# Kernel optimization log

Hardware: AMD Instinct MI355X
Metric: run time of the kernel (lower is better)

## Reference

```python
import jax, jax.numpy as jnp
import numpy as np
from jax import lax

B, N, C = 4, 20000, 256
NUM_VIEW = 300
NUM_SAMPLE = 1024
EPS_BN = 1e-5


def _grasp_views(n=NUM_VIEW):
    # graspnetAPI generate_grasp_views: spiral points on unit sphere
    phi = (np.sqrt(5.0) - 1.0) / 2.0
    i = np.arange(n)
    z = (2.0 * i + 1.0) / n - 1.0
    r = np.sqrt(np.maximum(1.0 - z * z, 0.0))
    x = r * np.cos(2.0 * np.pi * i * phi)
    y = r * np.sin(2.0 * np.pi * i * phi)
    return jnp.asarray(np.stack([x, y, z], axis=1).astype(np.float32))  # [300,3]

_TEMPLATE_VIEWS = _grasp_views()


def _conv1x1(x, w, b):
    # Conv1d with kernel_size=1: x [B,Cin,N], w [Cout,Cin], b [Cout]
    return jnp.einsum('oc,bcn->bon', w, x) + b[None, :, None]


def _bn_eval(x, g, be, m, v):
    # BatchNorm1d in eval mode (running stats)
    scale = g / jnp.sqrt(v + EPS_BN)
    return x * scale[None, :, None] + (be - m * scale)[None, :, None]


def _masked_fps(xyz, mask, n_samples):
    # Equivalent to compacting valid points, running torch furthest_point_sample,
    # and mapping indices back: run FPS on the full set with invalid points pinned
    # to -inf min-distance so they are never selected. Start = first valid index
    # (index 0 of the compacted set). Tie-breaking matches (order preserved).
    first = jnp.argmax(mask, axis=1)                      # [B]
    init_d = jnp.where(mask, jnp.float32(1e10), -jnp.inf)  # [B,N]

    def step(carry, _):
        dists, last = carry
        p = jnp.take_along_axis(xyz, last[:, None, None], axis=1)  # [B,1,3]
        d = jnp.sum((xyz - p) ** 2, axis=-1)                       # [B,N]
        dists = jnp.minimum(dists, d)
        nxt = jnp.argmax(dists, axis=1)
        return (dists, nxt), nxt

    _, rest = lax.scan(step, (init_d, first), None, length=n_samples - 1)
    return jnp.concatenate([first[None, :], rest], axis=0).T  # [B,S] int


def _viewpoint_to_matrix(towards):
    # batch_viewpoint_params_to_matrix with batch_angle = 0 => R1 = I
    ax = towards  # [M,3]
    ay = jnp.stack([-ax[:, 1], ax[:, 0], jnp.zeros_like(ax[:, 0])], axis=-1)
    deg = jnp.sum(ay * ay, axis=-1, keepdims=True) == 0
    ay = jnp.where(deg, jnp.array([0.0, 1.0, 0.0], dtype=ax.dtype), ay)
    nx = ax / jnp.linalg.norm(ax, axis=-1, keepdims=True)
    ny = ay / jnp.linalg.norm(ay, axis=-1, keepdims=True)
    nz = jnp.cross(nx, ny)
    return jnp.stack([nx, ny, nz], axis=-1)  # [M,3,3], axes as columns


def setup_inputs() -> dict:
    key = jax.random.key(0)
    ks = jax.random.split(key, 18)

    def w(k, shape, s=0.05):
        return jax.random.normal(k, shape, jnp.float32) * s

    return dict(
        seed_xyz=jax.random.normal(ks[0], (B, N, 3), jnp.float32),
        seed_features=jax.random.normal(ks[1], (B, C, N), jnp.float32),
        gh_w1=w(ks[2], (C, C)), gh_b1=w(ks[3], (C,), 0.01),
        gh_g=1.0 + 0.1 * jax.random.normal(ks[4], (C,), jnp.float32),
        gh_be=w(ks[5], (C,), 0.01),
        gh_m=w(ks[6], (C,), 0.1),
        gh_v=jax.random.uniform(ks[7], (C,), jnp.float32, 0.5, 1.5),
        gh_w2=w(ks[8], (3, C)), gh_b2=w(ks[9], (3,), 0.01),
        c1_w=w(ks[10], (C, C)), c1_b=w(ks[11], (C,), 0.01),
        bn_g=1.0 + 0.1 * jax.random.normal(ks[12], (C,), jnp.float32),
        bn_b=w(ks[13], (C,), 0.01),
        bn_m=w(ks[14], (C,), 0.1),
        bn_v=jax.random.uniform(ks[15], (C,), jnp.float32, 0.5, 1.5),
        c2_w=w(ks[16], (3, C)), c2_b=w(ks[17], (3,), 0.01),
    )


def reference(seed_xyz, seed_features, gh_w1, gh_b1, gh_g, gh_be, gh_m, gh_v,
              gh_w2, gh_b2, c1_w, c1_b, bn_g, bn_b, bn_m, bn_v, c2_w, c2_b):
    # graspable head: conv-BN-ReLU-conv -> [B,3,N]
    h = jax.nn.relu(_bn_eval(_conv1x1(seed_features, gh_w1, gh_b1), gh_g, gh_be, gh_m, gh_v))
    graspable = _conv1x1(h, gh_w2, gh_b2)
    objectness_score = graspable[:, :2]          # [B,2,N]
    graspness_score = graspable[:, 2]            # [B,N]

    obj_mask = jnp.argmax(objectness_score, axis=1) == 1
    gmask = (graspness_score > 0.1) & obj_mask   # [B,N] bool

    graspable_inds = _masked_fps(seed_xyz, gmask, NUM_SAMPLE)            # [B,S]
    graspable_xyz = jnp.take_along_axis(seed_xyz, graspable_inds[:, :, None], axis=1)   # [B,S,3]
    graspable_features = jnp.take_along_axis(seed_features, graspable_inds[:, None, :], axis=2)  # [B,C,S]
    fp2_graspness = jnp.take_along_axis(graspness_score, graspable_inds, axis=1)        # [B,S]

    f = jax.nn.relu(_bn_eval(_conv1x1(graspable_features, c1_w, c1_b), bn_g, bn_b, bn_m, bn_v))
    vp_xyz = jnp.transpose(_conv1x1(f, c2_w, c2_b), (0, 2, 1))  # [B,S,3]

    # cosine similarity against 300 template views (torch clamps each norm at 1e-8)
    vn = vp_xyz / jnp.maximum(jnp.linalg.norm(vp_xyz, axis=-1, keepdims=True), 1e-8)
    tn = _TEMPLATE_VIEWS / jnp.maximum(jnp.linalg.norm(_TEMPLATE_VIEWS, axis=-1, keepdims=True), 1e-8)
    cos = jnp.einsum('bsd,vd->bsv', vn, tn)      # [B,S,300]
    top_view_inds = jnp.argmax(cos, axis=2)      # [B,S]

    vp_rot = _viewpoint_to_matrix(-vp_xyz.reshape(-1, 3)).reshape(B, NUM_SAMPLE, 3, 3)

    return (objectness_score, graspness_score, graspable_xyz, graspable_inds,
            graspable_features, fp2_graspness, vp_xyz, top_view_inds, vp_rot)
```

## Files before the change

### kernel.cpp

```cpp
#include <hip/hip_runtime.h>
#include <hip/hip_bf16.h>
#include <math.h>

static constexpr int BB = 4;
static constexpr int NN = 20000;
static constexpr int CC = 256;
static constexpr int SS = 1024;
static constexpr int NV = 300;

static constexpr size_t O0 = 0;
static constexpr size_t O1 = O0 + (size_t)BB*2*NN;
static constexpr size_t O2 = O1 + (size_t)BB*NN;
static constexpr size_t O3 = O2 + (size_t)BB*SS*3;
static constexpr size_t O4 = O3 + (size_t)BB*SS;
static constexpr size_t O5 = O4 + (size_t)BB*CC*SS;
static constexpr size_t O6 = O5 + (size_t)BB*SS;
static constexpr size_t O7 = O6 + (size_t)BB*SS*3;
static constexpr size_t O8 = O7 + (size_t)BB*SS;

typedef float v2f __attribute__((ext_vector_type(2)));

static constexpr int TN = 64;
static constexpr int KC = 32;
static constexpr int SW_LD = 260;
static constexpr int PS_LD = 68;

static constexpr int G1_TN  = 64;
static constexpr int G1_KC  = 16;
static constexpr int G1_LD  = 260;
static constexpr int G1_BUF = G1_KC*G1_LD + G1_KC*G1_TN;

__global__ __launch_bounds__(256, 2) void gemm_fused(
    const float* __restrict__ X,
    const float* __restrict__ W1, const float* __restrict__ B1v,
    const float* __restrict__ Gv, const float* __restrict__ BEv,
    const float* __restrict__ Mv, const float* __restrict__ Vv,
    const float* __restrict__ W2, const float* __restrict__ B2v,
    float* __restrict__ o0, float* __restrict__ o1)
{
    __shared__ alignas(16) float smem[2*G1_BUF];
    float* psum = smem;
    float* gout = smem + 3*32*PS_LD;

    const int t  = threadIdx.x;
    const int b  = blockIdx.y;
    const int n0 = blockIdx.x * G1_TN;
    const int tm = t & 31;
    const int tn = t >> 5;
    const float* Xb = X + (size_t)b * CC * NN;
    const bool full = (n0 + G1_TN <= NN);

    v2f acc2[8][4];
#pragma unroll
    for (int i = 0; i < 8; ++i)
#pragma unroll
        for (int jp = 0; jp < 4; ++jp) acc2[i][jp] = (v2f){0.f, 0.f};

    float4 wreg[4];
    float4 xreg;

    auto stage_load = [&](int k0) {
#pragma unroll
        for (int r = 0; r < 4; ++r) {
            int f  = r*1024 + t*4;
            int m  = f >> 4;
            int kk = f & 15;
            wreg[r] = *(const float4*)&W1[(size_t)m*CC + k0 + kk];
        }
        int fx = t*4;
        int kk = fx >> 6;
        int j  = fx & 63;
        if (full) {
            xreg = *(const float4*)&Xb[(size_t)(k0+kk)*NN + n0 + j];
        } else {
            float tmp[4];
#pragma unroll
            for (int u = 0; u < 4; ++u) {
                int col = n0 + j + u;
                tmp[u] = (col < NN) ? Xb[(size_t)(k0+kk)*NN + col] : 0.f;
            }
            xreg = make_float4(tmp[0], tmp[1], tmp[2], tmp[3]);
        }
    };

    auto stage_write = [&](float* sWb, float* sFb) {
#pragma unroll
        for (int r = 0; r < 4; ++r) {
            int f  = r*1024 + t*4;
            int m  = f >> 4;
            int kk = f & 15;
            float tmp[4] = {wreg[r].x, wreg[r].y, wreg[r].z, wreg[r].w};
#pragma unroll
            for (int u = 0; u < 4; ++u)
                sWb[(kk+u)*G1_LD + m] = tmp[u];
        }
        int fx = t*4;
        int kk = fx >> 6;
        int j  = fx & 63;
        *(float4*)&sFb[kk*G1_TN + j] = xreg;
    };

    stage_load(0);
    stage_write(smem, smem + G1_KC*G1_LD);
    __syncthreads();

    for (int c = 0; c < CC/G1_KC; ++c) {
        const int cur = c & 1;
        float* base_cur = smem + cur*G1_BUF;
        float* base_nxt = smem + (cur^1)*G1_BUF;

        if (c + 1 < CC/G1_KC) stage_load((c+1)*G1_KC);

        const float* sWc = base_cur;
        const float* sFc = base_cur + G1_KC*G1_LD;
#pragma unroll 8
        for (int kk = 0; kk < G1_KC; ++kk) {
            const float4 a0 = *(const float4*)(sWc + kk*G1_LD + tm*8);
            const float4 a1 = *(const float4*)(sWc + kk*G1_LD + tm*8 + 4);
            const float4 f0 = *(const float4*)(sFc + kk*G1_TN + tn*8);
            const float4 f1 = *(const float4*)(sFc + kk*G1_TN + tn*8 + 4);
            float av[8] = {a0.x,a0.y,a0.z,a0.w,a1.x,a1.y,a1.z,a1.w};
            v2f bv2[4] = {{f0.x,f0.y},{f0.z,f0.w},{f1.x,f1.y},{f1.z,f1.w}};
#pragma unroll
            for (int i = 0; i < 8; ++i) {
                v2f ai = {av[i], av[i]};
#pragma unroll
                for (int jp = 0; jp < 4; ++jp)
                    acc2[i][jp] += ai * bv2[jp];
            }
        }

        if (c + 1 < CC/G1_KC) stage_write(base_nxt, base_nxt + G1_KC*G1_LD);
        __syncthreads();
    }

    float part[3][8];
#pragma unroll
    for (int r = 0; r < 3; ++r)
#pragma unroll
        for (int j = 0; j < 8; ++j) part[r][j] = 0.f;

#pragma unroll
    for (int i = 0; i < 8; ++i) {
        int m = tm*8 + i;
        float scale = __fdiv_rn(Gv[m], __fsqrt_rn(__fadd_rn(Vv[m], 1e-5f)));
        float shift = __fsub_rn(BEv[m], __fmul_rn(Mv[m], scale));
        float w0 = W2[m], w1 = W2[CC + m], w2 = W2[2*CC + m];
        float b1m = B1v[m];
#pragma unroll
        for (int j = 0; j < 8; ++j) {
            float x = __fadd_rn(acc2[i][j>>1][j&1], b1m);
            float y = __fadd_rn(__fmul_rn(x, scale), shift);
            float h = y > 0.f ? y : 0.f;
            part[0][j] = fmaf(w0, h, part[0][j]);
            part[1][j] = fmaf(w1, h, part[1][j]);
            part[2][j] = fmaf(w2, h, part[2][j]);
        }
    }
#pragma unroll
    for (int r = 0; r < 3; ++r) {
        float4 p0 = {part[r][0], part[r][1], part[r][2], part[r][3]};
        float4 p1 = {part[r][4], part[r][5], part[r][6], part[r][7]};
        *(float4*)(psum + (r*32 + tm)*PS_LD + tn*8)     = p0;
        *(float4*)(psum + (r*32 + tm)*PS_LD + tn*8 + 4) = p1;
    }
    __syncthreads();
    if (t < 192) {
        int r = t >> 6, col = t & 63;
        float s = 0.f;
#pragma unroll
        for (int w = 0; w < 32; ++w) s = __fadd_rn(s, psum[(r*32 + w)*PS_LD + col]);
        float tot = __fadd_rn(s, B2v[r]);
        gout[r*64 + col] = tot;
    }
    __syncthreads();
    if (t < 64) {
        int n = n0 + t;
        if (n < NN) {
            o0[(size_t)b*2*NN + n]      = gout[t];
            o0[(size_t)b*2*NN + NN + n] = gout[64 + t];
            o1[(size_t)b*NN + n]        = gout[128 + t];
        }
    }
}

static constexpr int FPS_T = 256;
static constexpr int KAMAX = 20;
static constexpr int CAPA  = FPS_T * KAMAX;

template<int CTRL>
__device__ __forceinline__ unsigned long long dpp_umax(unsigned long long k) {
    int lo = __builtin_amdgcn_update_dpp(0, (int)(unsigned)k,         CTRL, 0xf, 0xf, false);
    int hi = __builtin_amdgcn_update_dpp(0, (int)(unsigned)(k >> 32), CTRL, 0xf, 0xf, false);
    unsigned long long ok = ((unsigned long long)(unsigned)hi << 32) | (unsigned)lo;
    return ok > k ? ok : k;
}

__device__ __forceinline__ unsigned long long wave_umax_dpp(unsigned long long k) {
    k = dpp_umax<0x111>(k);
    k = dpp_umax<0x112>(k);
    k = dpp_umax<0x114>(k);
    k = dpp_umax<0x118>(k);
    k = dpp_umax<0x142>(k);
    k = dpp_umax<0x143>(k);
    return k;
}

__device__ __forceinline__ unsigned long long pack_key(float v, int i) {
    unsigned long long k = (((unsigned long long)__float_as_uint(v)) << 32)
                         | (unsigned long long)(0xFFFFFFFFu - (unsigned)i);
    return (v == -INFINITY) ? 0ull : k;
}

template<int KP>
__device__ __forceinline__ void fps_scan_loop(
    int cnt, const float* __restrict__ sxyz,
    unsigned long long (*swk)[4], int* __restrict__ whist)
{
#pragma clang fp contract(off)
    const int t = threadIdx.x;
    const int wave = t >> 6, lane = t & 63;

    v2f X2[KP], Y2[KP], Z2[KP], D2[KP];
#pragma unroll
    for (int jp = 0; jp < KP; ++jp) {
        int g0 = t + ((2*jp) << 8);
        int g1 = g0 + 256;
        bool v0 = g0 < cnt, v1 = g1 < cnt;
        float4 wa = v0 ? *(const float4*)&sxyz[g0*4] : make_float4(0.f,0.f,0.f,0.f);
        float4 wb = v1 ? *(const float4*)&sxyz[g1*4] : make_float4(0.f,0.f,0.f,0.f);
        X2[jp][0] = wa.x; X2[jp][1] = wb.x;
        Y2[jp][0] = wa.y; Y2[jp][1] = wb.y;
        Z2[jp][0] = wa.z; Z2[jp][1] = wb.z;
        D2[jp][0] = v0 ? 1e10f : -INFINITY;
        D2[jp][1] = v1 ? 1e10f : -INFINITY;
    }

    float px = sxyz[0], py = sxyz[1], pz = sxyz[2];

    for (int it = 1; it < SS; ++it) {
        float bv = -INFINITY; int bi = 0x7fffffff;
#pragma unroll
        for (int jp = 0; jp < KP; ++jp) {
            v2f dx = X2[jp] - px;
            v2f dy = Y2[jp] - py;
            v2f dz = Z2[jp] - pz;
            v2f xx = dx*dx, yy = dy*dy;
            v2f sxy = xx + yy;
            v2f zz = dz*dz;
            v2f dd = sxy + zz;
            float dn0 = fminf(D2[jp][0], dd[0]);
            float dn1 = fminf(D2[jp][1], dd[1]);
            D2[jp][0] = dn0;
            D2[jp][1] = dn1;
            if (dn0 > bv) { bv = dn0; bi = t + ((2*jp)   << 8); }
            if (dn1 > bv) { bv = dn1; bi = t + ((2*jp+1) << 8); }
        }
        unsigned long long key = wave_umax_dpp(pack_key(bv, bi));
        int par = it & 1;
        if (lane == 63) swk[par][wave] = key;
        __syncthreads();
        const ulonglong2* kp = (const ulonglong2*)&swk[par][0];
        ulonglong2 kA = kp[0], kB = kp[1];
        unsigned long long m0 = kA.x > kA.y ? kA.x : kA.y;
        unsigned long long m1 = kB.x > kB.y ? kB.x : kB.y;
        unsigned long long best = m0 > m1 ? m0 : m1;
        int wi = (int)(0xFFFFFFFFu - (unsigned)(best & 0xFFFFFFFFull));
        float4 w4 = *(const float4*)&sxyz[wi*4];
        px = w4.x; py = w4.y; pz = w4.z;
        if (t == 0) whist[it] = wi;
    }
}

__global__ __launch_bounds__(256, 1) void mega_kernel(
    const float* __restrict__ xyz, const float* __restrict__ feats,
    const float* __restrict__ o0, const float* __restrict__ o1,
    const float* __restrict__ c1w, const float* __restrict__ c1b,
    const float* __restrict__ bng, const float* __restrict__ bnb,
    const float* __restrict__ bnm, const float* __restrict__ bnv,
    const float* __restrict__ c2w, const float* __restrict__ c2b,
    int* __restrict__ corig, float* __restrict__ cxg,
    float* __restrict__ cyg, float* __restrict__ czg,
    float* __restrict__ o2, float* __restrict__ o3, float* __restrict__ o4,
    float* __restrict__ o5, float* __restrict__ o6, float* __restrict__ o7,
    float* __restrict__ o8, int* __restrict__ indsp, int* __restrict__ donep)
{
    __shared__ alignas(16) char sm[86272];
    const int t = threadIdx.x;
    const int wave = t >> 6, lane = t & 63;

    if (blockIdx.x < BB) {
        const int b = blockIdx.x;
        const size_t bofs = (size_t)b*NN;
        float* sxyz = (float*)sm;
        int*   whist = (int*)(sm + 81920);
        unsigned long long (*swk)[4] = (unsigned long long (*)[4])(sm + 86016);
        int*   wsum  = (int*)(sm + 86080);
        int*   smisc = (int*)(sm + 86096);

        if (t == 0) smisc[0] = 0;
        __syncthreads();
        const float* ob0 = o0 + (size_t)b*2*NN;
        const float* ob1 = o1 + (size_t)b*NN;
        for (int base = 0; base < NN; base += 256) {
            int i = base + t;
            bool valid = i < NN;
            float g1 = valid ? ob1[i]      : 0.f;
            float v0 = valid ? ob0[i]      : 0.f;
            float v1 = valid ? ob0[NN + i] : 0.f;
            bool m = valid && (g1 > 0.1f) && (v1 > v0);
            unsigned long long bal = __ballot(m);
            int pre = __popcll(bal & ((1ull << lane) - 1ull));
            if (lane == 0) wsum[wave] = __popcll(bal);
            __syncthreads();
            int offs = smisc[0];
            int tilesum = wsum[0] + wsum[1] + wsum[2] + wsum[3];
            for (int ww = 0; ww < wave; ++ww) offs += wsum[ww];
            if (m) {
                int pos = offs + pre;
                float x = xyz[(bofs + i)*3 + 0];
                float y = xyz[(bofs + i)*3 + 1];
                float z = xyz[(bofs + i)*3 + 2];
                corig[bofs + pos] = i;
                cxg[bofs + pos] = x; cyg[bofs + pos] = y; czg[bofs + pos] = z;
                if (pos < CAPA) {
                    float4 w4 = {x, y, z, 0.f};
                    *(float4*)&sxyz[pos*4] = w4;
                }
            }
            __syncthreads();
            if (t == 0) smisc[0] += tilesum;
        }
        __syncthreads();
        const int cnt = smisc[0];

        float* o3b = o3 + (size_t)b*SS;
        int*   oib = indsp + (size_t)b*SS;

        if (cnt <= 0) {
            for (int s = t; s < SS; s += FPS_T) { o3b[s] = 0.f; oib[s] = 0; }
            __syncthreads();
            if (t == 0) {
                __threadfence();
                __hip_atomic_fetch_add(donep, 1, __ATOMIC_RELEASE, __HIP_MEMORY_SCOPE_AGENT);
            }
            return;
        }

        if (t == 0) whist[0] = 0;
        __syncthreads();

        if (cnt <= CAPA) {
            int kat2 = ((cnt + 255) >> 8);
            kat2 = (kat2 + 1) & ~1;
            int kpn = kat2 >> 1;
            switch (kpn) {
                case 1:  fps_scan_loop<1 >(cnt, sxyz, swk, whist); break;
                case 2:  fps_scan_loop<2 >(cnt, sxyz, swk, whist); break;
                case 3:  fps_scan_loop<3 >(cnt, sxyz, swk, whist); break;
                case 4:  fps_scan_loop<4 >(cnt, sxyz, swk, whist); break;
                case 5:  fps_scan_loop<5 >(cnt, sxyz, swk, whist); break;
                case 6:  fps_scan_loop<6 >(cnt, sxyz, swk, whist); break;
                case 7:  fps_scan_loop<7 >(cnt, sxyz, swk, whist); break;
                case 8:  fps_scan_loop<8 >(cnt, sxyz, swk, whist); break;
                case 9:  fps_scan_loop<9 >(cnt, sxyz, swk, whist); break;
                default: fps_scan_loop<10>(cnt, sxyz, swk, whist); break;
            }
        } else {
            float* Dl = sxyz;
            for (int g = t; g < cnt; g += FPS_T) Dl[g] = 1e10f;
            __syncthreads();
            float px = cxg[bofs], py = cyg[bofs], pz = czg[bofs];
            for (int it = 1; it < SS; ++it) {
                float bv = -INFINITY; int bi = 0x7fffffff;
                for (int g = t; g < cnt; g += FPS_T) {
                    float dx = __fsub_rn(cxg[bofs + g], px);
                    float dy = __fsub_rn(cyg[bofs + g], py);
                    float dz = __fsub_rn(czg[bofs + g], pz);
                    float d  = __fadd_rn(__fadd_rn(__fmul_rn(dx,dx), __fmul_rn(dy,dy)), __fmul_rn(dz,dz));
                    float dn = fminf(Dl[g], d);
                    Dl[g] = dn;
                    if (dn > bv) { bv = dn; bi = g; }
                }
                unsigned long long key = wave_umax_dpp(pack_key(bv, bi));
                int par = it & 1;
                if (lane == 63) swk[par][wave] = key;
                __syncthreads();
                const ulonglong2* kp = (const ulonglong2*)&swk[par][0];
                ulonglong2 kA = kp[0], kB = kp[1];
                unsigned long long m0 = kA.x > kA.y ? kA.x : kA.y;
                unsigned long long m1 = kB.x > kB.y ? kB.x : kB.y;
                unsigned long long best = m0 > m1 ? m0 : m1;
                int wi = (int)(0xFFFFFFFFu - (unsigned)(best & 0xFFFFFFFFull));
                px = cxg[bofs + wi]; py = cyg[bofs + wi]; pz = czg[bofs + wi];
                if (t == 0) whist[it] = wi;
            }
        }

        __syncthreads();
        for (int s = t; s < SS; s += FPS_T) {
            int wi  = whist[s];
            int org = corig[bofs + wi];
            oib[s] = org;
            o3b[s] = (float)org;
        }
        __syncthreads();
        if (t == 0) {
            __threadfence();
            __hip_atomic_fetch_add(donep, 1, __ATOMIC_RELEASE, __HIP_MEMORY_SCOPE_AGENT);
        }
        return;
    }

    {
        int* smisc = (int*)(sm + 86096);
        if (t == 0) smisc[1] = 0;
        __syncthreads();
        float a = 1.0f + (float)t * 1e-6f, bmul = 1.0000001f, c = 0.f;
        for (int iter = 0; iter < (1 << 22); ++iter) {
#pragma unroll
            for (int u = 0; u < 16; ++u) c = fmaf(a, bmul, c);
            __builtin_amdgcn_s_sleep(8);
            if (t == 0 && (iter & 7) == 0) {
                if (__hip_atomic_load(donep, __ATOMIC_RELAXED, __HIP_MEMORY_SCOPE_AGENT) >= BB)
                    *(volatile int*)&smisc[1] = 1;
            }
            if (*(volatile int*)&smisc[1]) break;
        }
        ((volatile float*)sm)[32 + (t & 31)] = c;
        __syncthreads();
        (void)__hip_atomic_load(donep, __ATOMIC_ACQUIRE, __HIP_MEMORY_SCOPE_AGENT);
    }

    const int wid = blockIdx.x - BB;

    if (wid < 64) {
        const int bi = wid >> 4;
        const int n0 = (wid & 15) << 6;
        float* sW   = (float*)sm;
        float* sF   = (float*)(sm + KC*SW_LD*4);
        float* psum = (float*)sm;
        float* gout = (float*)(sm + 3*32*PS_LD*4);
        float* tv   = (float*)(sm + KC*SW_LD*4);
        int*   sIdx = (int*)(sm + 81920);

        if (t < 64) sIdx[t] = indsp[(bi << 10) + n0 + t];
        __syncthreads();

        const int tm = t & 31;
        const int tn = t >> 5;

        float acc[8][8];
#pragma unroll
        for (int i = 0; i < 8; ++i)
#pragma unroll
            for (int j = 0; j < 8; ++j) acc[i][j] = 0.f;

        for (int k0 = 0; k0 < CC; k0 += KC) {
#pragma unroll
            for (int r = 0; r < (CC*KC)/256; ++r) {
                int idx = r*256 + t;
                int m  = idx >> 5;
                int kk = idx & 31;
                sW[kk*SW_LD + m] = c1w[m*CC + k0 + kk];
            }
#pragma unroll
            for (int r = 0; r < (KC*TN)/256; ++r) {
                int idx = r*256 + t;
                int kk = idx >> 6;
                int j  = idx & 63;
                sF[kk*TN + j] = feats[((size_t)bi*CC + k0 + kk)*NN + sIdx[j]];
            }
            __syncthreads();
#pragma unroll 8
            for (int kk = 0; kk < KC; ++kk) {
                const float4 a0 = *(const float4*)(sW + kk*SW_LD + tm*8);
                const float4 a1 = *(const float4*)(sW + kk*SW_LD + tm*8 + 4);
                const float4 f0 = *(const float4*)(sF + kk*TN + tn*8);
                const float4 f1 = *(const float4*)(sF + kk*TN + tn*8 + 4);
                float av[8] = {a0.x,a0.y,a0.z,a0.w,a1.x,a1.y,a1.z,a1.w};
                float bv[8] = {f0.x,f0.y,f0.z,f0.w,f1.x,f1.y,f1.z,f1.w};
#pragma unroll
                for (int i = 0; i < 8; ++i)
#pragma unroll
                    for (int j = 0; j < 8; ++j)
                        acc[i][j] = fmaf(av[i], bv[j], acc[i][j]);
            }
            __syncthreads();
        }

        float part[3][8];
#pragma unroll
        for (int r = 0; r < 3; ++r)
#pragma unroll
            for (int j = 0; j < 8; ++j) part[r][j] = 0.f;

#pragma unroll
        for (int i = 0; i < 8; ++i) {
            int m = tm*8 + i;
            float scale = __fdiv_rn(bng[m], __fsqrt_rn(__fadd_rn(bnv[m], 1e-5f)));
            float shift = __fsub_rn(bnb[m], __fmul_rn(bnm[m], scale));
            float w0 = c2w[m], w1 = c2w[CC + m], w2 = c2w[2*CC + m];
            float b1m = c1b[m];
#pragma unroll
            for (int j = 0; j < 8; ++j) {
                float x = __fadd_rn(acc[i][j], b1m);
                float y = __fadd_rn(__fmul_rn(x, scale), shift);
                float h = y > 0.f ? y : 0.f;
                part[0][j] = fmaf(w0, h, part[0][j]);
                part[1][j] = fmaf(w1, h, part[1][j]);
                part[2][j] = fmaf(w2, h, part[2][j]);
            }
        }
#pragma unroll
        for (int r = 0; r < 3; ++r) {
            float4 p0 = {part[r][0], part[r][1], part[r][2], part[r][3]};
            float4 p1 = {part[r][4], part[r][5], part[r][6], part[r][7]};
            *(float4*)(psum + (r*32 + tm)*PS_LD + tn*8)     = p0;
            *(float4*)(psum + (r*32 + tm)*PS_LD + tn*8 + 4) = p1;
        }
        __syncthreads();
        if (t < 192) {
            int r = t >> 6, col = t & 63;
            float s = 0.f;
#pragma unroll
            for (int w = 0; w < 32; ++w) s = __fadd_rn(s, psum[(r*32 + w)*PS_LD + col]);
            float tot = __fadd_rn(s, c2b[r]);
            gout[r*64 + col] = tot;
            o6[((size_t)bi*SS + n0 + col)*3 + r] = tot;
        }
        __syncthreads();
        for (int i = t; i < NV; i += 256) {
            double phi = (sqrt(5.0) - 1.0) * 0.5;
            double zd  = (2.0*(double)i + 1.0)/300.0 - 1.0;
            double rr  = sqrt(fmax(1.0 - zd*zd, 0.0));
            double ang = 2.0 * 3.14159265358979323846 * (double)i * phi;
            float fx = (float)(rr * cos(ang));
            float fy = (float)(rr * sin(ang));
            float fz = (float)zd;
            float nr = __fsqrt_rn(__fadd_rn(__fadd_rn(__fmul_rn(fx,fx), __fmul_rn(fy,fy)), __fmul_rn(fz,fz)));
            float dn = fmaxf(nr, 1e-8f);
            tv[i]       = __fdiv_rn(fx, dn);
            tv[NV + i]  = __fdiv_rn(fy, dn);
            tv[2*NV + i]= __fdiv_rn(fz, dn);
        }
        __syncthreads();
        if (t < 64) {
            int col = t;
            int sg = bi*SS + n0 + col;
            float vx = gout[col], vy = gout[64 + col], vz = gout[128 + col];

            float nr = __fsqrt_rn(__fadd_rn(__fadd_rn(__fmul_rn(vx,vx), __fmul_rn(vy,vy)), __fmul_rn(vz,vz)));
            float dn = fmaxf(nr, 1e-8f);
            float ux = __fdiv_rn(vx, dn), uy = __fdiv_rn(vy, dn), uz = __fdiv_rn(vz, dn);
            float best = -INFINITY; int bidx = 0;
            for (int v = 0; v < NV; ++v) {
                float cde = __fadd_rn(__fadd_rn(__fmul_rn(ux, tv[v]), __fmul_rn(uy, tv[NV+v])), __fmul_rn(uz, tv[2*NV+v]));
                if (cde > best) { best = cde; bidx = v; }
            }
            o7[sg] = (float)bidx;

            float axx = -vx, axy = -vy, axz = -vz;
            float ayx = vy, ayy = -vx, ayz = 0.f;
            float s2 = __fadd_rn(__fadd_rn(__fmul_rn(ayx,ayx), __fmul_rn(ayy,ayy)), 0.f);
            if (s2 == 0.f) { ayx = 0.f; ayy = 1.f; ayz = 0.f; }
            float an = __fsqrt_rn(__fadd_rn(__fadd_rn(__fmul_rn(axx,axx), __fmul_rn(axy,axy)), __fmul_rn(axz,axz)));
            float nx0 = __fdiv_rn(axx, an), nx1 = __fdiv_rn(axy, an), nx2 = __fdiv_rn(axz, an);
            float bn2 = __fsqrt_rn(__fadd_rn(__fadd_rn(__fmul_rn(ayx,ayx), __fmul_rn(ayy,ayy)), __fmul_rn(ayz,ayz)));
            float ny0 = __fdiv_rn(ayx, bn2), ny1 = __fdiv_rn(ayy, bn2), ny2 = __fdiv_rn(ayz, bn2);
            float nz0 = __fsub_rn(__fmul_rn(nx1, ny2), __fmul_rn(nx2, ny1));
            float nz1 = __fsub_rn(__fmul_rn(nx2, ny0), __fmul_rn(nx0, ny2));
            float nz2 = __fsub_rn(__fmul_rn(nx0, ny1), __fmul_rn(nx1, ny0));
            size_t o = (size_t)sg * 9;
            o8[o+0] = nx0; o8[o+1] = ny0; o8[o+2] = nz0;
            o8[o+3] = nx1; o8[o+4] = ny1; o8[o+5] = nz1;
            o8[o+6] = nx2; o8[o+7] = ny2; o8[o+8] = nz2;
        }
    } else {
        const int NQ = (BB*CC*SS) / 4;
        for (int q = (wid - 64)*256 + t; q < NQ; q += 188*256) {
            int e = q << 2;
            int b = e >> 18;
            int r = e & ((1 << 18) - 1);
            int c = r >> 10;
            int s = r & 1023;
            int4 i4 = *(const int4*)&indsp[(b << 10) + s];
            const float* fb = feats + ((size_t)b*CC + c)*NN;
            float4 v = { fb[i4.x], fb[i4.y], fb[i4.z], fb[i4.w] };
            *(float4*)&o4[e] = v;
            if (c == 0) {
                const float* gb = o1 + (size_t)b*NN;
                float4 g4 = { gb[i4.x], gb[i4.y], gb[i4.z], gb[i4.w] };
                *(float4*)&o5[(b << 10) + s] = g4;
                const float* xb = xyz + (size_t)b*NN*3;
                float o2buf[12];
                int ii[4] = { i4.x, i4.y, i4.z, i4.w };
#pragma unroll
                for (int k = 0; k < 4; ++k) {
                    o2buf[k*3+0] = xb[(size_t)ii[k]*3 + 0];
                    o2buf[k*3+1] = xb[(size_t)ii[k]*3 + 1];
                    o2buf[k*3+2] = xb[(size_t)ii[k]*3 + 2];
                }
                float* dst = o2 + ((size_t)(b << 10) + s)*3;
                *(float4*)&dst[0] = *(float4*)&o2buf[0];
                *(float4*)&dst[4] = *(float4*)&o2buf[4];
                *(float4*)&dst[8] = *(float4*)&o2buf[8];
            }
        }
    }
}

extern "C" void kernel_launch(void* const* d_in, const int* in_sizes, int n_in,
                              void* d_out, int out_size, void* d_ws, size_t ws_size,
                              hipStream_t stream) {
    const float* xyz   = (const float*)d_in[0];
    const float* feats = (const float*)d_in[1];
    const float* gh_w1 = (const float*)d_in[2];
    const float* gh_b1 = (const float*)d_in[3];
    const float* gh_g  = (const float*)d_in[4];
    const float* gh_be = (const float*)d_in[5];
    const float* gh_m  = (const float*)d_in[6];
    const float* gh_v  = (const float*)d_in[7];
    const float* gh_w2 = (const float*)d_in[8];
    const float* gh_b2 = (const float*)d_in[9];
    const float* c1_w  = (const float*)d_in[10];
    const float* c1_b  = (const float*)d_in[11];
    const float* bn_g  = (const float*)d_in[12];
    const float* bn_b  = (const float*)d_in[13];
    const float* bn_m  = (const float*)d_in[14];
    const float* bn_v  = (const float*)d_in[15];
    const float* c2_w  = (const float*)d_in[16];
    const float* c2_b  = (const float*)d_in[17];

    float* out = (float*)d_out;
    float* o0 = out + O0;
    float* o1 = out + O1;
    float* o2 = out + O2;
    float* o3 = out + O3;
    float* o4 = out + O4;
    float* o5 = out + O5;
    float* o6 = out + O6;
    float* o7 = out + O7;
    float* o8 = out + O8;

    char* ws = (char*)d_ws;
    size_t off = 0;
    auto take = [&](size_t bytes) -> char* {
        char* p = ws + off;
        off = (off + bytes + 255) & ~(size_t)255;
        return p;
    };
    int*   corig = (int*)take((size_t)BB*NN*4);
    float* cx    = (float*)take((size_t)BB*NN*4);
    float* cy    = (float*)take((size_t)BB*NN*4);
    float* cz    = (float*)take((size_t)BB*NN*4);
    int*   indsp = (int*)take((size_t)BB*SS*4);
    int*   donep = (int*)take(64);

    gemm_fused<<<dim3((NN + G1_TN - 1)/G1_TN, BB), 256, 0, stream>>>(
        feats, gh_w1, gh_b1, gh_g, gh_be, gh_m, gh_v, gh_w2, gh_b2, o0, o1);

    hipMemsetAsync(donep, 0, 4, stream);
    mega_kernel<<<dim3(256), 256, 0, stream>>>(
        xyz, feats, o0, o1,
        c1_w, c1_b, bn_g, bn_b, bn_m, bn_v, c2_w, c2_b,
        corig, cx, cy, cz,
        o2, o3, o4, o5, o6, o7, o8, indsp, donep);
}
```

Measured before the change: 944.2 us.

## Widen first GEMM tile to 128 columns and pipeline the gathered second GEMM

The first conv GEMM tile grows from 64 to 128 columns per block, with 128 accumulators per thread, and its epilogue now runs in two halves. The goal is more weight reuse and fewer blocks. The post-FPS gathered GEMM is rebuilt as a double-buffered, register-prefetched pipeline using packed v2f FMAs, and it preloads the first weight slice before the inter-block spin wait. The risks are higher register pressure in the first GEMM, which may lower occupancy under launch_bounds(256,2), and a changed shared-memory scratch offset for the spin value.

```diff
diff --git a/kernel.cpp b/kernel.cpp
--- a/kernel.cpp
+++ b/kernel.cpp
@@ -20,12 +20,11 @@
 
 typedef float v2f __attribute__((ext_vector_type(2)));
 
-static constexpr int TN = 64;
 static constexpr int KC = 32;
 static constexpr int SW_LD = 260;
 static constexpr int PS_LD = 68;
 
-static constexpr int G1_TN  = 64;
+static constexpr int G1_TN  = 128;
 static constexpr int G1_KC  = 16;
 static constexpr int G1_LD  = 260;
 static constexpr int G1_BUF = G1_KC*G1_LD + G1_KC*G1_TN;
@@ -40,24 +39,23 @@
 {
     __shared__ alignas(16) float smem[2*G1_BUF];
     float* psum = smem;
-    float* gout = smem + 3*32*PS_LD;
 
     const int t  = threadIdx.x;
     const int b  = blockIdx.y;
     const int n0 = blockIdx.x * G1_TN;
     const int tm = t & 31;
-    const int tn = t >> 5;
+    const int tj = t >> 5;
     const float* Xb = X + (size_t)b * CC * NN;
     const bool full = (n0 + G1_TN <= NN);
 
-    v2f acc2[8][4];
+    v2f acc2[8][8];
 #pragma unroll
     for (int i = 0; i < 8; ++i)
 #pragma unroll
-        for (int jp = 0; jp < 4; ++jp) acc2[i][jp] = (v2f){0.f, 0.f};
+        for (int jp = 0; jp < 8; ++jp) acc2[i][jp] = (v2f){0.f, 0.f};
 
     float4 wreg[4];
-    float4 xreg;
+    float4 xr0, xr1;
 
     auto stage_load = [&](int k0) {
 #pragma unroll
@@ -67,23 +65,29 @@
             int kk = f & 15;
             wreg[r] = *(const float4*)&W1[(size_t)m*CC + k0 + kk];
         }
-        int fx = t*4;
-        int kk = fx >> 6;
-        int j  = fx & 63;
+        int fx = t*8;
+        int kk = fx >> 7;
+        int j  = fx & 127;
         if (full) {
-            xreg = *(const float4*)&Xb[(size_t)(k0+kk)*NN + n0 + j];
+            xr0 = *(const float4*)&Xb[(size_t)(k0+kk)*NN + n0 + j];
+            xr1 = *(const float4*)&Xb[(size_t)(k0+kk)*NN + n0 + j + 4];
         } else {
-            float tmp[4];
+            float ta[4], tb[4];
 #pragma unroll
             for (int u = 0; u < 4; ++u) {
-                int col = n0 + j + u;
-                tmp[u] = (col < NN) ? Xb[(size_t)(k0+kk)*NN + col] : 0.f;
-            }
-            xreg = make_float4(tmp[0], tmp[1], tmp[2], tmp[3]);
+                int c0 = n0 + j + u;
+                int c1 = n0 + j + 4 + u;
+                ta[u] = (c0 < NN) ? Xb[(size_t)(k0+kk)*NN + c0] : 0.f;
+                tb[u] = (c1 < NN) ? Xb[(size_t)(k0+kk)*NN + c1] : 0.f;
+            }
+            xr0 = make_float4(ta[0], ta[1], ta[2], ta[3]);
+            xr1 = make_float4(tb[0], tb[1], tb[2], tb[3]);
         }
     };
 
-    auto stage_write = [&](float* sWb, float* sFb) {
+    auto stage_write = [&](float* base) {
+        float* sWb = base;
+        float* sFb = base + G1_KC*G1_LD;
 #pragma unroll
         for (int r = 0; r < 4; ++r) {
             int f  = r*1024 + t*4;
@@ -94,14 +98,15 @@
             for (int u = 0; u < 4; ++u)
                 sWb[(kk+u)*G1_LD + m] = tmp[u];
         }
-        int fx = t*4;
-        int kk = fx >> 6;
-        int j  = fx & 63;
-        *(float4*)&sFb[kk*G1_TN + j] = xreg;
+        int fx = t*8;
+        int kk = fx >> 7;
+        int j  = fx & 127;
+        *(float4*)&sFb[kk*G1_TN + j]     = xr0;
+        *(float4*)&sFb[kk*G1_TN + j + 4] = xr1;
     };
 
     stage_load(0);
-    stage_write(smem, smem + G1_KC*G1_LD);
+    stage_write(smem);
     __syncthreads();
 
     for (int c = 0; c < CC/G1_KC; ++c) {
@@ -117,70 +122,74 @@
         for (int kk = 0; kk < G1_KC; ++kk) {
             const float4 a0 = *(const float4*)(sWc + kk*G1_LD + tm*8);
             const float4 a1 = *(const float4*)(sWc + kk*G1_LD + tm*8 + 4);
-            const float4 f0 = *(const float4*)(sFc + kk*G1_TN + tn*8);
-            const float4 f1 = *(const float4*)(sFc + kk*G1_TN + tn*8 + 4);
+            const float4 f0 = *(const float4*)(sFc + kk*G1_TN + tj*16);
+            const float4 f1 = *(const float4*)(sFc + kk*G1_TN + tj*16 + 4);
+            const float4 f2 = *(const float4*)(sFc + kk*G1_TN + tj*16 + 8);
+            const float4 f3 = *(const float4*)(sFc + kk*G1_TN + tj*16 + 12);
             float av[8] = {a0.x,a0.y,a0.z,a0.w,a1.x,a1.y,a1.z,a1.w};
-            v2f bv2[4] = {{f0.x,f0.y},{f0.z,f0.w},{f1.x,f1.y},{f1.z,f1.w}};
+            v2f bv2[8] = {{f0.x,f0.y},{f0.z,f0.w},{f1.x,f1.y},{f1.z,f1.w},
+                          {f2.x,f2.y},{f2.z,f2.w},{f3.x,f3.y},{f3.z,f3.w}};
 #pragma unroll
             for (int i = 0; i < 8; ++i) {
                 v2f ai = {av[i], av[i]};
 #pragma unroll
-                for (int jp = 0; jp < 4; ++jp)
+                for (int jp = 0; jp < 8; ++jp)
                     acc2[i][jp] += ai * bv2[jp];
             }
         }
 
-        if (c + 1 < CC/G1_KC) stage_write(base_nxt, base_nxt + G1_KC*G1_LD);
+        if (c + 1 < CC/G1_KC) stage_write(base_nxt);
         __syncthreads();
     }
 
-    float part[3][8];
-#pragma unroll
-    for (int r = 0; r < 3; ++r)
-#pragma unroll
-        for (int j = 0; j < 8; ++j) part[r][j] = 0.f;
-
-#pragma unroll
-    for (int i = 0; i < 8; ++i) {
-        int m = tm*8 + i;
-        float scale = __fdiv_rn(Gv[m], __fsqrt_rn(__fadd_rn(Vv[m], 1e-5f)));
-        float shift = __fsub_rn(BEv[m], __fmul_rn(Mv[m], scale));
-        float w0 = W2[m], w1 = W2[CC + m], w2 = W2[2*CC + m];
-        float b1m = B1v[m];
-#pragma unroll
-        for (int j = 0; j < 8; ++j) {
-            float x = __fadd_rn(acc2[i][j>>1][j&1], b1m);
-            float y = __fadd_rn(__fmul_rn(x, scale), shift);
-            float h = y > 0.f ? y : 0.f;
-            part[0][j] = fmaf(w0, h, part[0][j]);
-            part[1][j] = fmaf(w1, h, part[1][j]);
-            part[2][j] = fmaf(w2, h, part[2][j]);
-        }
-    }
-#pragma unroll
-    for (int r = 0; r < 3; ++r) {
-        float4 p0 = {part[r][0], part[r][1], part[r][2], part[r][3]};
-        float4 p1 = {part[r][4], part[r][5], part[r][6], part[r][7]};
-        *(float4*)(psum + (r*32 + tm)*PS_LD + tn*8)     = p0;
-        *(float4*)(psum + (r*32 + tm)*PS_LD + tn*8 + 4) = p1;
-    }
-    __syncthreads();
-    if (t < 192) {
-        int r = t >> 6, col = t & 63;
-        float s = 0.f;
-#pragma unroll
-        for (int w = 0; w < 32; ++w) s = __fadd_rn(s, psum[(r*32 + w)*PS_LD + col]);
-        float tot = __fadd_rn(s, B2v[r]);
-        gout[r*64 + col] = tot;
-    }
-    __syncthreads();
-    if (t < 64) {
-        int n = n0 + t;
-        if (n < NN) {
-            o0[(size_t)b*2*NN + n]      = gout[t];
-            o0[(size_t)b*2*NN + NN + n] = gout[64 + t];
-            o1[(size_t)b*NN + n]        = gout[128 + t];
-        }
+    for (int h = 0; h < 2; ++h) {
+        if ((tj >> 2) == h) {
+            float part[3][16];
+#pragma unroll
+            for (int r = 0; r < 3; ++r)
+#pragma unroll
+                for (int j = 0; j < 16; ++j) part[r][j] = 0.f;
+#pragma unroll
+            for (int i = 0; i < 8; ++i) {
+                int m = tm*8 + i;
+                float scale = __fdiv_rn(Gv[m], __fsqrt_rn(__fadd_rn(Vv[m], 1e-5f)));
+                float shift = __fsub_rn(BEv[m], __fmul_rn(Mv[m], scale));
+                float w0 = W2[m], w1 = W2[CC + m], w2 = W2[2*CC + m];
+                float b1m = B1v[m];
+#pragma unroll
+                for (int j = 0; j < 16; ++j) {
+                    float x = __fadd_rn(acc2[i][j>>1][j&1], b1m);
+                    float y = __fadd_rn(__fmul_rn(x, scale), shift);
+                    float hv = y > 0.f ? y : 0.f;
+                    part[0][j] = fmaf(w0, hv, part[0][j]);
+                    part[1][j] = fmaf(w1, hv, part[1][j]);
+                    part[2][j] = fmaf(w2, hv, part[2][j]);
+                }
+            }
+            int tq = tj & 3;
+#pragma unroll
+            for (int r = 0; r < 3; ++r)
+#pragma unroll
+                for (int q = 0; q < 4; ++q) {
+                    float4 p = {part[r][4*q], part[r][4*q+1], part[r][4*q+2], part[r][4*q+3]};
+                    *(float4*)(psum + (r*32 + tm)*PS_LD + tq*16 + q*4) = p;
+                }
+        }
+        __syncthreads();
+        if (t < 192) {
+            int r = t >> 6, col = t & 63;
+            float s = 0.f;
+#pragma unroll
+            for (int w = 0; w < 32; ++w) s = __fadd_rn(s, psum[(r*32 + w)*PS_LD + col]);
+            float tot = __fadd_rn(s, B2v[r]);
+            int n = n0 + h*64 + col;
+            if (n < NN) {
+                if (r == 0)      o0[(size_t)b*2*NN + n]      = tot;
+                else if (r == 1) o0[(size_t)b*2*NN + NN + n] = tot;
+                else             o1[(size_t)b*NN + n]        = tot;
+            }
+        }
+        __syncthreads();
     }
 }
 
@@ -412,6 +421,19 @@
         return;
     }
 
+    const int wid = blockIdx.x - BB;
+
+    float4 g2w[4];
+    if (wid < 64) {
+#pragma unroll
+        for (int r = 0; r < 4; ++r) {
+            int f  = r*1024 + t*4;
+            int m  = f >> 4;
+            int kk = f & 15;
+            g2w[r] = *(const float4*)&c1w[(size_t)m*CC + kk];
+        }
+    }
+
     {
         int* smisc = (int*)(sm + 86096);
         if (t == 0) smisc[1] = 0;
@@ -427,65 +449,104 @@
             }
             if (*(volatile int*)&smisc[1]) break;
         }
-        ((volatile float*)sm)[32 + (t & 31)] = c;
+        ((volatile float*)(sm + 86144))[t & 31] = c;
         __syncthreads();
         (void)__hip_atomic_load(donep, __ATOMIC_ACQUIRE, __HIP_MEMORY_SCOPE_AGENT);
     }
-
-    const int wid = blockIdx.x - BB;
 
     if (wid < 64) {
         const int bi = wid >> 4;
         const int n0 = (wid & 15) << 6;
-        float* sW   = (float*)sm;
-        float* sF   = (float*)(sm + KC*SW_LD*4);
-        float* psum = (float*)sm;
+        constexpr int G2_KC  = 16;
+        constexpr int G2_LD  = 260;
+        constexpr int G2_TN  = 64;
+        constexpr int G2_BUF = G2_KC*G2_LD + G2_KC*G2_TN;
+
+        float* smf  = (float*)sm;
+        float* psum = smf;
         float* gout = (float*)(sm + 3*32*PS_LD*4);
         float* tv   = (float*)(sm + KC*SW_LD*4);
-        int*   sIdx = (int*)(sm + 81920);
-
-        if (t < 64) sIdx[t] = indsp[(bi << 10) + n0 + t];
-        __syncthreads();
-
-        const int tm = t & 31;
-        const int tn = t >> 5;
-
-        float acc[8][8];
+
+        const int tm  = t & 31;
+        const int tn  = t >> 5;
+        const int kk0 = t >> 4;
+        const int j0  = (t*4) & 63;
+
+        const int4 sidx4 = *(const int4*)&indsp[(bi << 10) + n0 + j0];
+        const size_t frow_base = (size_t)bi * CC;
+
+        v2f acc2[8][4];
 #pragma unroll
         for (int i = 0; i < 8; ++i)
 #pragma unroll
-            for (int j = 0; j < 8; ++j) acc[i][j] = 0.f;
-
-        for (int k0 = 0; k0 < CC; k0 += KC) {
-#pragma unroll
-            for (int r = 0; r < (CC*KC)/256; ++r) {
-                int idx = r*256 + t;
-                int m  = idx >> 5;
-                int kk = idx & 31;
-                sW[kk*SW_LD + m] = c1w[m*CC + k0 + kk];
-            }
-#pragma unroll
-            for (int r = 0; r < (KC*TN)/256; ++r) {
-                int idx = r*256 + t;
-                int kk = idx >> 6;
-                int j  = idx & 63;
-                sF[kk*TN + j] = feats[((size_t)bi*CC + k0 + kk)*NN + sIdx[j]];
-            }
-            __syncthreads();
+            for (int jp = 0; jp < 4; ++jp) acc2[i][jp] = (v2f){0.f, 0.f};
+
+        float4 wreg[4] = {g2w[0], g2w[1], g2w[2], g2w[3]};
+        float4 xreg;
+
+        auto loadW = [&](int k0) {
+#pragma unroll
+            for (int r = 0; r < 4; ++r) {
+                int f  = r*1024 + t*4;
+                int m  = f >> 4;
+                int kk = f & 15;
+                wreg[r] = *(const float4*)&c1w[(size_t)m*CC + k0 + kk];
+            }
+        };
+        auto loadF = [&](int k0) {
+            const float* fb = feats + (frow_base + k0 + kk0)*NN;
+            xreg.x = fb[sidx4.x];
+            xreg.y = fb[sidx4.y];
+            xreg.z = fb[sidx4.z];
+            xreg.w = fb[sidx4.w];
+        };
+        auto stage_write = [&](float* base) {
+            float* sWb = base;
+            float* sFb = base + G2_KC*G2_LD;
+#pragma unroll
+            for (int r = 0; r < 4; ++r) {
+                int f  = r*1024 + t*4;
+                int m  = f >> 4;
+                int kk = f & 15;
+                float tmp[4] = {wreg[r].x, wreg[r].y, wreg[r].z, wreg[r].w};
+#pragma unroll
+                for (int u = 0; u < 4; ++u)
+                    sWb[(kk+u)*G2_LD + m] = tmp[u];
+            }
+            *(float4*)&sFb[kk0*G2_TN + j0] = xreg;
+        };
+
+        loadF(0);
+        stage_write(smf);
+        __syncthreads();
+
+        for (int c = 0; c < CC/G2_KC; ++c) {
+            const int cur = c & 1;
+            float* bcur = smf + cur*G2_BUF;
+            float* bnxt = smf + (cur^1)*G2_BUF;
+
+            if (c + 1 < CC/G2_KC) { loadW((c+1)*G2_KC); loadF((c+1)*G2_KC); }
+
+            const float* sWc = bcur;
+            const float* sFc = bcur + G2_KC*G2_LD;
 #pragma unroll 8
-            for (int kk = 0; kk < KC; ++kk) {
-                const float4 a0 = *(const float4*)(sW + kk*SW_LD + tm*8);
-                const float4 a1 = *(const float4*)(sW + kk*SW_LD + tm*8 + 4);
-                const float4 f0 = *(const float4*)(sF + kk*TN + tn*8);
-                const float4 f1 = *(const float4*)(sF + kk*TN + tn*8 + 4);
+            for (int kk = 0; kk < G2_KC; ++kk) {
+                const float4 a0 = *(const float4*)(sWc + kk*G2_LD + tm*8);
+                const float4 a1 = *(const float4*)(sWc + kk*G2_LD + tm*8 + 4);
+                const float4 f0 = *(const float4*)(sFc + kk*G2_TN + tn*8);
+                const float4 f1 = *(const float4*)(sFc + kk*G2_TN + tn*8 + 4);
                 float av[8] = {a0.x,a0.y,a0.z,a0.w,a1.x,a1.y,a1.z,a1.w};
-                float bv[8] = {f0.x,f0.y,f0.z,f0.w,f1.x,f1.y,f1.z,f1.w};
-#pragma unroll
-                for (int i = 0; i < 8; ++i)
-#pragma unroll
-                    for (int j = 0; j < 8; ++j)
-                        acc[i][j] = fmaf(av[i], bv[j], acc[i][j]);
-            }
+                v2f bv2[4] = {{f0.x,f0.y},{f0.z,f0.w},{f1.x,f1.y},{f1.z,f1.w}};
+#pragma unroll
+                for (int i = 0; i < 8; ++i) {
+                    v2f ai = {av[i], av[i]};
+#pragma unroll
+                    for (int jp = 0; jp < 4; ++jp)
+                        acc2[i][jp] += ai * bv2[jp];
+                }
+            }
+
+            if (c + 1 < CC/G2_KC) stage_write(bnxt);
             __syncthreads();
         }
 
@@ -504,7 +565,7 @@
             float b1m = c1b[m];
 #pragma unroll
             for (int j = 0; j < 8; ++j) {
-                float x = __fadd_rn(acc[i][j], b1m);
+                float x = __fadd_rn(acc2[i][j>>1][j&1], b1m);
                 float y = __fadd_rn(__fmul_rn(x, scale), shift);
                 float h = y > 0.f ? y : 0.f;
                 part[0][j] = fmaf(w0, h, part[0][j]);
```

After: 960.5 us. No clear change (+1.7%).
